# Kernel tuning notes

Hardware: AMD Instinct MI355X
Metric: run time of the kernel (lower is better)

## Reference

```python
import jax, jax.numpy as jnp
import numpy as np

B, S, IN, D, H, FF, L = 16, 1000, 32, 512, 8, 2048, 6
DK = D // H
EPS = 1e-5


def setup_inputs() -> dict:
    key = jax.random.key(0)
    ks = iter(jax.random.split(key, 64))
    def w(shape, s=0.02):
        return jax.random.normal(next(ks), shape, dtype=jnp.float32) * s
    inp = {
        'x': jax.random.normal(next(ks), (B, S, IN), dtype=jnp.float32),
        # input projection
        'Win': w((IN, D)), 'b_in': jnp.zeros((D,), jnp.float32),
        # per-layer attention weights (stacked over L layers)
        'Wq': w((L, D, D)), 'bq': jnp.zeros((L, D), jnp.float32),
        'Wk': w((L, D, D)), 'bk': jnp.zeros((L, D), jnp.float32),
        'Wv': w((L, D, D)), 'bv': jnp.zeros((L, D), jnp.float32),
        'Wo': w((L, D, D)), 'bo': jnp.zeros((L, D), jnp.float32),
        # per-layer feed-forward
        'W1': w((L, D, FF)), 'b1': jnp.zeros((L, FF), jnp.float32),
        'W2': w((L, FF, D)), 'b2': jnp.zeros((L, D), jnp.float32),
        # per-layer layernorms
        'ln1_g': jnp.ones((L, D), jnp.float32), 'ln1_b': jnp.zeros((L, D), jnp.float32),
        'ln2_g': jnp.ones((L, D), jnp.float32), 'ln2_b': jnp.zeros((L, D), jnp.float32),
        # final encoder norm
        'lnf_g': jnp.ones((D,), jnp.float32), 'lnf_b': jnp.zeros((D,), jnp.float32),
        # feature extraction head: D -> D/2 -> D/4
        'Wf1': w((D, D // 2)), 'bf1': jnp.zeros((D // 2,), jnp.float32),
        'Wf2': w((D // 2, D // 4)), 'bf2': jnp.zeros((D // 4,), jnp.float32),
        # reconstruction head: D/4 -> D/2 -> D -> IN
        'Wr1': w((D // 4, D // 2)), 'br1': jnp.zeros((D // 2,), jnp.float32),
        'Wr2': w((D // 2, D)), 'br2': jnp.zeros((D,), jnp.float32),
        'Wr3': w((D, IN)), 'br3': jnp.zeros((IN,), jnp.float32),
        # anomaly head: D/4 -> D/8 -> 1
        'Wa1': w((D // 4, D // 8)), 'ba1': jnp.zeros((D // 8,), jnp.float32),
        'Wa2': w((D // 8, 1)), 'ba2': jnp.zeros((1,), jnp.float32),
    }
    return inp


def _layernorm(x, g, b):
    m = jnp.mean(x, axis=-1, keepdims=True)
    v = jnp.var(x, axis=-1, keepdims=True)
    return (x - m) * jax.lax.rsqrt(v + EPS) * g + b


def _pos_encoding(seq_len, d_model):
    pos = jnp.arange(seq_len, dtype=jnp.float32)[:, None]
    div = jnp.exp(jnp.arange(0, d_model, 2, dtype=jnp.float32) * (-np.log(10000.0) / d_model))
    pe = jnp.zeros((seq_len, d_model), jnp.float32)
    pe = pe.at[:, 0::2].set(jnp.sin(pos * div))
    pe = pe.at[:, 1::2].set(jnp.cos(pos * div))
    return pe


def _encoder(h, Wq, bq, Wk, bk, Wv, bv, Wo, bo, W1, b1, W2, b2,
             ln1_g, ln1_b, ln2_g, ln2_b, lnf_g, lnf_b):
    h = h + _pos_encoding(h.shape[1], D)[None]
    scale = 1.0 / np.sqrt(DK)
    for i in range(L):
        # multi-head self-attention
        q = (h @ Wq[i] + bq[i]).reshape(B, S, H, DK).transpose(0, 2, 1, 3)
        k = (h @ Wk[i] + bk[i]).reshape(B, S, H, DK).transpose(0, 2, 1, 3)
        v = (h @ Wv[i] + bv[i]).reshape(B, S, H, DK).transpose(0, 2, 1, 3)
        scores = jnp.einsum('bhsd,bhtd->bhst', q, k) * scale  # [B,H,S,S]
        attn = jax.nn.softmax(scores, axis=-1)
        ctx = jnp.einsum('bhst,bhtd->bhsd', attn, v)
        ctx = ctx.transpose(0, 2, 1, 3).reshape(B, S, D)
        attn_out = ctx @ Wo[i] + bo[i]
        h = _layernorm(h + attn_out, ln1_g[i], ln1_b[i])
        # feed-forward
        ff = jax.nn.relu(h @ W1[i] + b1[i]) @ W2[i] + b2[i]
        h = _layernorm(h + ff, ln2_g[i], ln2_b[i])
    return _layernorm(h, lnf_g, lnf_b)


def reference(x, Win, b_in, Wq, bq, Wk, bk, Wv, bv, Wo, bo, W1, b1, W2, b2,
              ln1_g, ln1_b, ln2_g, ln2_b, lnf_g, lnf_b,
              Wf1, bf1, Wf2, bf2, Wr1, br1, Wr2, br2, Wr3, br3,
              Wa1, ba1, Wa2, ba2):
    h = x @ Win + b_in  # [B,S,D]
    h = _encoder(h, Wq, bq, Wk, bk, Wv, bv, Wo, bo, W1, b1, W2, b2,
                 ln1_g, ln1_b, ln2_g, ln2_b, lnf_g, lnf_b)
    feat = jax.nn.relu(h @ Wf1 + bf1) @ Wf2 + bf2  # [B,S,D/4]
    recon = jax.nn.relu(jax.nn.relu(feat @ Wr1 + br1) @ Wr2 + br2) @ Wr3 + br3  # [B,S,IN]
    anomaly = jax.nn.sigmoid(jax.nn.relu(feat @ Wa1 + ba1) @ Wa2 + ba2)  # [B,S,1]
    return recon, anomaly
```

## Files before the change

### kernel.cpp

```cpp
#include <hip/hip_runtime.h>
#include <hip/hip_bf16.h>
#include <math.h>

#define B_  16
#define S_  1000
#define IN_ 32
#define D_  512
#define H_  8
#define FF_ 2048
#define L_  6
#define DK_ 64
#define M_  (B_ * S_)
#define SP_ 1024

typedef __bf16 bf16x8 __attribute__((ext_vector_type(8)));
typedef float  floatx4 __attribute__((ext_vector_type(4)));

#define FLAG_RELU 1
#define FLAG_BF16 2
#define FLAG_QKV  4

#define QSCALE 0.18033688011112042f

__device__ __forceinline__ void gll16(const __bf16* g, __bf16* l) {
    __builtin_amdgcn_global_load_lds(
        (const __attribute__((address_space(1))) unsigned int*)g,
        (__attribute__((address_space(3))) unsigned int*)l, 16, 0, 0);
}

__global__ __launch_bounds__(256) void gemm_mfma(
    const __bf16* __restrict__ A, const __bf16* __restrict__ BT,
    const float* __restrict__ bias, void* __restrict__ C,
    int M, int N, int K, int flags)
{
    __shared__ __bf16 Asm[128 * 32];
    __shared__ __bf16 Bsm[128 * 32];

    int tid  = threadIdx.x;
    int wave = tid >> 6;
    int lane = tid & 63;
    int bm = blockIdx.y * 128;
    int bn = blockIdx.x * 128;
    int wm = (wave & 1) * 64;
    int wn = (wave >> 1) * 64;
    int lm = lane & 15;
    int lq = lane >> 4;

    floatx4 acc[4][4] = {};

    int crow  = tid >> 2;
    int cpart = (tid & 3) * 8;
    const __bf16* ag0 = A + (size_t)(bm + crow) * K + cpart;
    const __bf16* ag1 = A + (size_t)(bm + 64 + crow) * K + cpart;
    __bf16* al0 = Asm + tid * 8;
    __bf16* al1 = Asm + 2048 + tid * 8;
    int nr0 = bn + crow, nr1 = bn + 64 + crow;
    const __bf16* bg0 = BT + (size_t)nr0 * K + cpart;
    const __bf16* bg1 = BT + (size_t)nr1 * K + cpart;
    __bf16* bl0 = Bsm + tid * 8;
    __bf16* bl1 = Bsm + 2048 + tid * 8;
    bool bv0 = nr0 < N, bv1 = nr1 < N;

    for (int k0 = 0; k0 < K; k0 += 32) {
        __syncthreads();
        gll16(ag0 + k0, al0);
        gll16(ag1 + k0, al1);
        if (bv0) gll16(bg0 + k0, bl0);
        if (bv1) gll16(bg1 + k0, bl1);
        __syncthreads();

        bf16x8 af[4], bf[4];
        #pragma unroll
        for (int i = 0; i < 4; ++i) {
            af[i] = *(const bf16x8*)&Asm[(wm + i * 16 + lm) * 32 + lq * 8];
            bf[i] = *(const bf16x8*)&Bsm[(wn + i * 16 + lm) * 32 + lq * 8];
        }
        #pragma unroll
        for (int i = 0; i < 4; ++i)
            #pragma unroll
            for (int j = 0; j < 4; ++j)
                acc[i][j] = __builtin_amdgcn_mfma_f32_16x16x32_bf16(
                    af[i], bf[j], acc[i][j], 0, 0, 0);
    }

    if (flags & FLAG_QKV) {
        int sec = bn >> 9;
        if (sec < 2) {
            __bf16* dst = (__bf16*)C + (sec ? (size_t)8192000 : 0);
            #pragma unroll
            for (int j = 0; j < 4; ++j) {
                int col = (bn & 511) + wn + j * 16 + lm;
                float bvv = bias[bn + wn + j * 16 + lm];
                #pragma unroll
                for (int i = 0; i < 4; ++i)
                    #pragma unroll
                    for (int r = 0; r < 4; ++r) {
                        int m = bm + wm + i * 16 + lq * 4 + r;
                        dst[(size_t)m * 512 + col] = (__bf16)(acc[i][j][r] + bvv);
                    }
            }
        } else {
            __bf16* vt = (__bf16*)C + (size_t)16384000;
            int bbq[4], s0[4];
            #pragma unroll
            for (int i = 0; i < 4; ++i) {
                int m0 = bm + wm + i * 16 + lq * 4;
                bbq[i] = m0 / 1000;
                s0[i]  = m0 - bbq[i] * 1000;
            }
            #pragma unroll
            for (int j = 0; j < 4; ++j) {
                int col = (bn & 511) + wn + j * 16 + lm;
                float bvv = bias[bn + wn + j * 16 + lm];
                int head = col >> 6, dk = col & 63;
                #pragma unroll
                for (int i = 0; i < 4; ++i) {
                    __bf16 t4[4];
                    #pragma unroll
                    for (int r = 0; r < 4; ++r) t4[r] = (__bf16)(acc[i][j][r] + bvv);
                    *(uint2*)(vt + ((size_t)(bbq[i] * H_ + head) * DK_ + dk) * SP_ + s0[i])
                        = *(uint2*)t4;
                }
            }
        }
        return;
    }

    #pragma unroll
    for (int j = 0; j < 4; ++j) {
        int n = bn + wn + j * 16 + lm;
        if (n >= N) continue;
        float bv = bias[n];
        #pragma unroll
        for (int i = 0; i < 4; ++i) {
            #pragma unroll
            for (int r = 0; r < 4; ++r) {
                int m = bm + wm + i * 16 + lq * 4 + r;
                float v = acc[i][j][r] + bv;
                if (flags & FLAG_RELU) v = fmaxf(v, 0.f);
                if (flags & FLAG_BF16) ((__bf16*)C)[(size_t)m * N + n] = (__bf16)v;
                else                   ((float*)C)[(size_t)m * N + n] = v;
            }
        }
    }
}

__device__ __forceinline__ void trans_tile(
    const float* __restrict__ src, __bf16* __restrict__ dst,
    int K, int N, float scale, int tx0, int ty0)
{
    __shared__ float t[32][33];
    int n0 = tx0 * 32, k0 = ty0 * 32;
    int tx = threadIdx.x & 31, ty = threadIdx.x >> 5;
    #pragma unroll
    for (int i = 0; i < 32; i += 8) {
        int k = k0 + ty + i, n = n0 + tx;
        t[ty + i][tx] = (k < K && n < N) ? src[(size_t)k * N + n] * scale : 0.f;
    }
    __syncthreads();
    #pragma unroll
    for (int i = 0; i < 32; i += 8) {
        int n = n0 + ty + i, k = k0 + tx;
        if (n < N && k < K) dst[(size_t)n * K + k] = (__bf16)t[tx][ty + i];
    }
}

__global__ __launch_bounds__(256) void transpose_qkvo(
    const float* __restrict__ Wq, const float* __restrict__ Wk,
    const float* __restrict__ Wv, const float* __restrict__ Wo,
    __bf16* __restrict__ WqkvT, __bf16* __restrict__ WoT)
{
    int l = blockIdx.z >> 2, which = blockIdx.z & 3;
    const float* src; __bf16* dst; float sc = 1.f;
    size_t so = (size_t)l * 512 * 512;
    if (which == 0)      { src = Wq + so; dst = WqkvT + (size_t)l * 1536 * 512; sc = QSCALE; }
    else if (which == 1) { src = Wk + so; dst = WqkvT + (size_t)l * 1536 * 512 + 512 * 512; }
    else if (which == 2) { src = Wv + so; dst = WqkvT + (size_t)l * 1536 * 512 + 1024 * 512; }
    else                 { src = Wo + so; dst = WoT + so; }
    trans_tile(src, dst, 512, 512, sc, blockIdx.x, blockIdx.y);
}

__global__ __launch_bounds__(256) void transpose_ffn(
    const float* __restrict__ W1, const float* __restrict__ W2,
    __bf16* __restrict__ W1T, __bf16* __restrict__ W2T)
{
    int l = blockIdx.z >> 1, which = blockIdx.z & 1;
    size_t so = (size_t)l * 512 * 2048;
    int K = which ? 2048 : 512, N = which ? 512 : 2048;
    if ((int)blockIdx.x >= N / 32 || (int)blockIdx.y >= K / 32) return;
    trans_tile((which ? W2 : W1) + so, (which ? W2T : W1T) + so,
               K, N, 1.f, blockIdx.x, blockIdx.y);
}

struct TDesc { const float* src; __bf16* dst; int K; int N; float scale; };
struct TDescArr { TDesc d[7]; };

__global__ __launch_bounds__(256) void transpose_misc(TDescArr ds)
{
    TDesc t = ds.d[blockIdx.z];
    if ((int)blockIdx.x * 32 >= t.N || (int)blockIdx.y * 32 >= t.K) return;
    trans_tile(t.src, t.dst, t.K, t.N, t.scale, blockIdx.x, blockIdx.y);
}

__global__ void cast_bf16(const float* __restrict__ src, __bf16* __restrict__ dst, int n)
{
    int i = blockIdx.x * 256 + threadIdx.x;
    if (i < n) dst[i] = (__bf16)src[i];
}

__global__ void concat_bias(const float* __restrict__ bq, const float* __restrict__ bk,
                            const float* __restrict__ bv, float* __restrict__ dst)
{
    int i = blockIdx.x * 256 + threadIdx.x;
    if (i >= L_ * 1536) return;
    int l = i / 1536, j = i - l * 1536;
    float v = (j < 512) ? bq[l * 512 + j] * QSCALE
            : (j < 1024) ? bk[l * 512 + j - 512]
                         : bv[l * 512 + j - 1024];
    dst[i] = v;
}

__global__ void add_pos_kernel(float* __restrict__ h, __bf16* __restrict__ hb)
{
    int idx = blockIdx.x * 256 + threadIdx.x;
    if (idx >= B_ * S_ * D_) return;
    int d = idx % D_;
    int s = (idx / D_) % S_;
    int two_i = d & ~1;
    float ang = (float)s * expf((float)two_i * (-9.210340371976184f / (float)D_));
    float v = h[idx] + ((d & 1) ? cosf(ang) : sinf(ang));
    h[idx] = v;
    hb[idx] = (__bf16)v;
}

#define AST 72

__global__ __launch_bounds__(256) void attn_mfma(
    const __bf16* __restrict__ q, const __bf16* __restrict__ k,
    const __bf16* __restrict__ vt, __bf16* __restrict__ ctx)
{
    const int id = blockIdx.x;
    const int w  = (id & 7) * 128 + (id >> 3);
    const int qt = w & 7, hh = (w >> 3) & 7, bb = w >> 6;

    const int tid = threadIdx.x;
    const int wave = tid >> 6, lane = tid & 63;
    const int lm = lane & 15, lq = lane >> 4;

    __shared__ __bf16 Ks[64 * AST];
    __shared__ __bf16 Vt[64 * AST];

    const size_t headbase = (size_t)bb * S_ * D_ + hh * DK_;
    const __bf16* kbase  = k + headbase;
    const __bf16* vtbase = vt + (size_t)(bb * H_ + hh) * DK_ * SP_;

    bf16x8 af[2][2] = {};
    #pragma unroll
    for (int iq = 0; iq < 2; ++iq) {
        int qrow = qt * 128 + wave * 32 + iq * 16 + lm;
        if (qrow < S_) {
            const __bf16* qp = q + headbase + (size_t)qrow * D_;
            af[iq][0] = *(const bf16x8*)(qp + lq * 8);
            af[iq][1] = *(const bf16x8*)(qp + 32 + lq * 8);
        }
    }

    floatx4 oacc[2][4] = {};
    floatx4 lacc[2] = {};

    bf16x8 ones8;
    #pragma unroll
    for (int j = 0; j < 8; ++j) ones8[j] = (__bf16)1.f;

    const int sr  = tid >> 3;
    const int sc8 = (tid & 7) * 8;
    const int colA = (sc8 & 32) | ((sc8 & 8) << 1) | ((sc8 & 16) >> 2);

    uint4 ku[2], vu[2];
    #pragma unroll
    for (int i = 0; i < 2; ++i) {
        int r = sr + i * 32;
        ku[i] = *(const uint4*)(kbase + (size_t)r * D_ + sc8);
        vu[i] = *(const uint4*)(vtbase + (size_t)r * SP_ + sc8);
    }

    for (int jt = 0; jt < 16; ++jt) {
        const int t0 = jt * 64;
        const bool tail = (jt == 15);

        __syncthreads();
        #pragma unroll
        for (int i = 0; i < 2; ++i) {
            int r = sr + i * 32;
            *(uint4*)&Ks[r * AST + sc8] = ku[i];
            uint2 vlo = make_uint2(vu[i].x, vu[i].y);
            uint2 vhi = make_uint2(vu[i].z, vu[i].w);
            *(uint2*)&Vt[r * AST + colA]     = vlo;
            *(uint2*)&Vt[r * AST + colA + 8] = vhi;
        }
        __syncthreads();

        if (jt < 15) {
            int t0n = t0 + 64;
            #pragma unroll
            for (int i = 0; i < 2; ++i) {
                int r = sr + i * 32;
                int trow = t0n + r;
                ku[i] = (trow < S_) ? *(const uint4*)(kbase + (size_t)trow * D_ + sc8)
                                    : make_uint4(0, 0, 0, 0);
                vu[i] = *(const uint4*)(vtbase + (size_t)r * SP_ + t0n + sc8);
            }
        }

        #pragma unroll
        for (int iq = 0; iq < 2; ++iq) {
            floatx4 sacc[4] = {};
            #pragma unroll
            for (int ks = 0; ks < 2; ++ks)
                #pragma unroll
                for (int jb = 0; jb < 4; ++jb) {
                    bf16x8 kf = *(const bf16x8*)&Ks[(jb * 16 + lm) * AST + ks * 32 + lq * 8];
                    sacc[jb] = __builtin_amdgcn_mfma_f32_16x16x32_bf16(
                        kf, af[iq][ks], sacc[jb], 0, 0, 0);
                }

            bf16x8 pf[2];
            if (!tail) {
                #pragma unroll
                for (int jb = 0; jb < 4; ++jb)
                    #pragma unroll
                    for (int r = 0; r < 4; ++r)
                        pf[jb >> 1][(jb & 1) * 4 + r] = (__bf16)exp2f(sacc[jb][r]);
            } else {
                #pragma unroll
                for (int jb = 0; jb < 4; ++jb)
                    #pragma unroll
                    for (int r = 0; r < 4; ++r) {
                        bool valid = (t0 + jb * 16 + lq * 4 + r) < S_;
                        pf[jb >> 1][(jb & 1) * 4 + r] =
                            valid ? (__bf16)exp2f(sacc[jb][r]) : (__bf16)0.f;
                    }
            }

            #pragma unroll
            for (int ks = 0; ks < 2; ++ks) {
                #pragma unroll
                for (int jb = 0; jb < 4; ++jb) {
                    bf16x8 bvf = *(const bf16x8*)&Vt[(jb * 16 + lm) * AST + ks * 32 + lq * 8];
                    oacc[iq][jb] = __builtin_amdgcn_mfma_f32_16x16x32_bf16(
                        pf[ks], bvf, oacc[iq][jb], 0, 0, 0);
                }
                lacc[iq] = __builtin_amdgcn_mfma_f32_16x16x32_bf16(
                    pf[ks], ones8, lacc[iq], 0, 0, 0);
            }
        }
    }

    #pragma unroll
    for (int iq = 0; iq < 2; ++iq) {
        float linv[4];
        #pragma unroll
        for (int r = 0; r < 4; ++r)
            linv[r] = 1.f / lacc[iq][r];
        #pragma unroll
        for (int jb = 0; jb < 4; ++jb)
            #pragma unroll
            for (int r = 0; r < 4; ++r) {
                int srow = qt * 128 + wave * 32 + iq * 16 + lq * 4 + r;
                if (srow < S_)
                    ctx[headbase + (size_t)srow * D_ + jb * 16 + lm] =
                        (__bf16)(oacc[iq][jb][r] * linv[r]);
            }
    }
}

__global__ __launch_bounds__(256) void ln_kernel(
    const float* __restrict__ x, const __bf16* __restrict__ delta,
    const float* __restrict__ g, const float* __restrict__ b,
    float* __restrict__ out, __bf16* __restrict__ outb, int has_delta)
{
    int row = blockIdx.x;
    int tid = threadIdx.x;
    __shared__ float red[256];

    const size_t base = (size_t)row * D_;
    float v0 = x[base + tid];
    float v1 = x[base + tid + 256];
    if (has_delta) {
        v0 += (float)delta[base + tid];
        v1 += (float)delta[base + tid + 256];
    }
    red[tid] = v0 + v1; __syncthreads();
    for (int o = 128; o > 0; o >>= 1) {
        if (tid < o) red[tid] += red[tid + o];
        __syncthreads();
    }
    float mean = red[0] * (1.f / D_);
    __syncthreads();
    float d0 = v0 - mean, d1 = v1 - mean;
    red[tid] = d0 * d0 + d1 * d1; __syncthreads();
    for (int o = 128; o > 0; o >>= 1) {
        if (tid < o) red[tid] += red[tid + o];
        __syncthreads();
    }
    float rstd = rsqrtf(red[0] * (1.f / D_) + 1e-5f);
    float o0 = d0 * rstd * g[tid]       + b[tid];
    float o1 = d1 * rstd * g[tid + 256] + b[tid + 256];
    out[base + tid]        = o0;
    out[base + tid + 256]  = o1;
    outb[base + tid]       = (__bf16)o0;
    outb[base + tid + 256] = (__bf16)o1;
}

__global__ __launch_bounds__(256) void a2_kernel(
    const float* __restrict__ a1, const float* __restrict__ Wa2,
    const float* __restrict__ ba2, float* __restrict__ out)
{
    int row = blockIdx.x * 4 + (threadIdx.x >> 6);
    int lane = threadIdx.x & 63;
    if (row >= M_) return;
    float p = a1[(size_t)row * 64 + lane] * Wa2[lane];
    for (int o = 32; o > 0; o >>= 1) p += __shfl_down(p, o, 64);
    if (lane == 0) out[row] = 1.f / (1.f + expf(-(p + ba2[0])));
}

extern "C" void kernel_launch(void* const* d_in, const int* in_sizes, int n_in,
                              void* d_out, int out_size, void* d_ws, size_t ws_size,
                              hipStream_t stream)
{
    const float* x     = (const float*)d_in[0];
    const float* Win   = (const float*)d_in[1];
    const float* b_in  = (const float*)d_in[2];
    const float* Wq    = (const float*)d_in[3];
    const float* bq    = (const float*)d_in[4];
    const float* Wk    = (const float*)d_in[5];
    const float* bk    = (const float*)d_in[6];
    const float* Wv    = (const float*)d_in[7];
    const float* bv    = (const float*)d_in[8];
    const float* Wo    = (const float*)d_in[9];
    const float* bo    = (const float*)d_in[10];
    const float* W1    = (const float*)d_in[11];
    const float* b1    = (const float*)d_in[12];
    const float* W2    = (const float*)d_in[13];
    const float* b2    = (const float*)d_in[14];
    const float* ln1_g = (const float*)d_in[15];
    const float* ln1_b = (const float*)d_in[16];
    const float* ln2_g = (const float*)d_in[17];
    const float* ln2_b = (const float*)d_in[18];
    const float* lnf_g = (const float*)d_in[19];
    const float* lnf_b = (const float*)d_in[20];
    const float* Wf1   = (const float*)d_in[21];
    const float* bf1   = (const float*)d_in[22];
    const float* Wf2   = (const float*)d_in[23];
    const float* bf2   = (const float*)d_in[24];
    const float* Wr1   = (const float*)d_in[25];
    const float* br1   = (const float*)d_in[26];
    const float* Wr2   = (const float*)d_in[27];
    const float* br2   = (const float*)d_in[28];
    const float* Wr3   = (const float*)d_in[29];
    const float* br3   = (const float*)d_in[30];
    const float* Wa1   = (const float*)d_in[31];
    const float* ba1   = (const float*)d_in[32];
    const float* Wa2   = (const float*)d_in[33];
    const float* ba2   = (const float*)d_in[34];

    float* recon_out   = (float*)d_out;
    float* anomaly_out = (float*)d_out + (size_t)M_ * IN_;

    char* ws = (char*)d_ws;
    float*  h    = (float*)(ws + 0);
    __bf16* tmpb = (__bf16*)(ws + 32768000);
    __bf16* hb   = (__bf16*)(ws + 65536000);
    __bf16* qb   = (__bf16*)(ws + 81920000);
    __bf16* kb   = (__bf16*)(ws + 98304000);
    __bf16* vtb  = (__bf16*)(ws + 114688000);
    __bf16* ctxb = (__bf16*)(ws + 131465216);
    __bf16* ffmid = qb;

    __bf16* t1b   = (__bf16*)(ws + 81920000);
    __bf16* featb = (__bf16*)(ws + 90112000);
    __bf16* r1b   = (__bf16*)(ws + 94208000);
    __bf16* r2b   = (__bf16*)(ws + 102400000);
    float*  a1b   = (float*)(ws + 118784000);

    size_t woff = 147849216;
    auto alloc_bf = [&](size_t elems) { __bf16* p = (__bf16*)(ws + woff); woff += elems * 2; return p; };
    __bf16* WinT  = alloc_bf(32 * 512);
    __bf16* WqkvT = alloc_bf((size_t)L_ * 1536 * 512);
    __bf16* WoT   = alloc_bf((size_t)L_ * 512 * 512);
    __bf16* W1T   = alloc_bf((size_t)L_ * 512 * 2048);
    __bf16* W2T   = alloc_bf((size_t)L_ * 2048 * 512);
    __bf16* Wf1T  = alloc_bf(512 * 256);
    __bf16* Wf2T  = alloc_bf(256 * 128);
    __bf16* Wr1T  = alloc_bf(128 * 256);
    __bf16* Wr2T  = alloc_bf(256 * 512);
    __bf16* Wr3T  = alloc_bf(512 * 32);
    __bf16* Wa1T  = alloc_bf(128 * 64);
    __bf16* xb    = alloc_bf((size_t)M_ * IN_);
    float*  bqkv  = (float*)(ws + woff);  woff += (size_t)L_ * 1536 * 4;

    dim3 blk(256);
    auto gg = [](int N) { return dim3((N + 127) / 128, M_ / 128); };

    hipLaunchKernelGGL(transpose_qkvo, dim3(16, 16, L_ * 4), blk, 0, stream,
                       Wq, Wk, Wv, Wo, WqkvT, WoT);
    hipLaunchKernelGGL(transpose_ffn, dim3(64, 64, L_ * 2), blk, 0, stream,
                       W1, W2, W1T, W2T);
    TDescArr misc;
    misc.d[0] = {Win, WinT, 32, 512, 1.f};
    misc.d[1] = {Wf1, Wf1T, 512, 256, 1.f};
    misc.d[2] = {Wf2, Wf2T, 256, 128, 1.f};
    misc.d[3] = {Wr1, Wr1T, 128, 256, 1.f};
    misc.d[4] = {Wr2, Wr2T, 256, 512, 1.f};
    misc.d[5] = {Wr3, Wr3T, 512, 32, 1.f};
    misc.d[6] = {Wa1, Wa1T, 128, 64, 1.f};
    hipLaunchKernelGGL(transpose_misc, dim3(16, 16, 7), blk, 0, stream, misc);
    hipLaunchKernelGGL(cast_bf16, dim3((M_ * IN_ + 255) / 256), blk, 0, stream,
                       x, xb, M_ * IN_);
    hipLaunchKernelGGL(concat_bias, dim3((L_ * 1536 + 255) / 256), blk, 0, stream,
                       bq, bk, bv, bqkv);

    hipLaunchKernelGGL(gemm_mfma, gg(D_), blk, 0, stream,
                       xb, WinT, b_in, (void*)h, M_, D_, IN_, 0);
    hipLaunchKernelGGL(add_pos_kernel, dim3((B_ * S_ * D_ + 255) / 256), blk, 0, stream,
                       h, hb);

    for (int l = 0; l < L_; ++l) {
        size_t wo = (size_t)l * 512 * 512;
        size_t fo = (size_t)l * 512 * 2048;

        hipLaunchKernelGGL(gemm_mfma, dim3(12, M_ / 128), blk, 0, stream,
                           hb, WqkvT + (size_t)l * 1536 * 512, bqkv + (size_t)l * 1536,
                           (void*)qb, M_, 1536, 512, FLAG_QKV);

        hipLaunchKernelGGL(attn_mfma, dim3(1024), blk, 0, stream,
                           qb, kb, vtb, ctxb);

        hipLaunchKernelGGL(gemm_mfma, gg(D_), blk, 0, stream,
                           ctxb, WoT + wo, bo + (size_t)l * D_, (void*)tmpb, M_, D_, D_,
                           FLAG_BF16);
        hipLaunchKernelGGL(ln_kernel, dim3(M_), blk, 0, stream,
                           h, tmpb, ln1_g + (size_t)l * D_, ln1_b + (size_t)l * D_, h, hb, 1);

        hipLaunchKernelGGL(gemm_mfma, gg(FF_), blk, 0, stream,
                           hb, W1T + fo, b1 + (size_t)l * FF_, (void*)ffmid, M_, FF_, D_,
                           FLAG_RELU | FLAG_BF16);
        hipLaunchKernelGGL(gemm_mfma, gg(D_), blk, 0, stream,
                           ffmid, W2T + fo, b2 + (size_t)l * D_, (void*)tmpb, M_, D_, FF_,
                           FLAG_BF16);
        hipLaunchKernelGGL(ln_kernel, dim3(M_), blk, 0, stream,
                           h, tmpb, ln2_g + (size_t)l * D_, ln2_b + (size_t)l * D_, h, hb, 1);
    }

    hipLaunchKernelGGL(ln_kernel, dim3(M_), blk, 0, stream,
                       h, nullptr, lnf_g, lnf_b, h, hb, 0);

    hipLaunchKernelGGL(gemm_mfma, gg(256), blk, 0, stream,
                       hb, Wf1T, bf1, (void*)t1b, M_, 256, 512, FLAG_RELU | FLAG_BF16);
    hipLaunchKernelGGL(gemm_mfma, gg(128), blk, 0, stream,
                       t1b, Wf2T, bf2, (void*)featb, M_, 128, 256, FLAG_BF16);

    hipLaunchKernelGGL(gemm_mfma, gg(256), blk, 0, stream,
                       featb, Wr1T, br1, (void*)r1b, M_, 256, 128, FLAG_RELU | FLAG_BF16);
    hipLaunchKernelGGL(gemm_mfma, gg(512), blk, 0, stream,
                       r1b, Wr2T, br2, (void*)r2b, M_, 512, 256, FLAG_RELU | FLAG_BF16);
    hipLaunchKernelGGL(gemm_mfma, gg(IN_), blk, 0, stream,
                       r2b, Wr3T, br3, (void*)recon_out, M_, IN_, 512, 0);

    hipLaunchKernelGGL(gemm_mfma, gg(64), blk, 0, stream,
                       featb, Wa1T, ba1, (void*)a1b, M_, 64, 128, FLAG_RELU);
    hipLaunchKernelGGL(a2_kernel, dim3((M_ + 3) / 4), blk, 0, stream,
                       a1b, Wa2, ba2, anomaly_out);
}
```

Measured before the change: 1.989 ms.

## Double-buffer GEMM LDS tiles with register prefetch instead of direct global-to-LDS loads

Replaces the global_load_lds path in the MFMA GEMM with register-staged loads into two LDS buffers. The next K-tile is fetched into registers while the current tile is consumed, which drops one barrier per iteration and overlaps global latency with MFMA work. This doubles LDS use and adds register pressure, and it gives up the direct global-to-LDS path.

Measured after the change: 1.959 ms. No clear change (-1.5%).

```diff
diff --git a/kernel.cpp b/kernel.cpp
--- a/kernel.cpp
+++ b/kernel.cpp
@@ -22,19 +22,13 @@
 
 #define QSCALE 0.18033688011112042f
 
-__device__ __forceinline__ void gll16(const __bf16* g, __bf16* l) {
-    __builtin_amdgcn_global_load_lds(
-        (const __attribute__((address_space(1))) unsigned int*)g,
-        (__attribute__((address_space(3))) unsigned int*)l, 16, 0, 0);
-}
-
 __global__ __launch_bounds__(256) void gemm_mfma(
     const __bf16* __restrict__ A, const __bf16* __restrict__ BT,
     const float* __restrict__ bias, void* __restrict__ C,
     int M, int N, int K, int flags)
 {
-    __shared__ __bf16 Asm[128 * 32];
-    __shared__ __bf16 Bsm[128 * 32];
+    __shared__ __bf16 Asm[2][128 * 32];
+    __shared__ __bf16 Bsm[2][128 * 32];
 
     int tid  = threadIdx.x;
     int wave = tid >> 6;
@@ -52,28 +46,37 @@
     int cpart = (tid & 3) * 8;
     const __bf16* ag0 = A + (size_t)(bm + crow) * K + cpart;
     const __bf16* ag1 = A + (size_t)(bm + 64 + crow) * K + cpart;
-    __bf16* al0 = Asm + tid * 8;
-    __bf16* al1 = Asm + 2048 + tid * 8;
     int nr0 = bn + crow, nr1 = bn + 64 + crow;
     const __bf16* bg0 = BT + (size_t)nr0 * K + cpart;
     const __bf16* bg1 = BT + (size_t)nr1 * K + cpart;
-    __bf16* bl0 = Bsm + tid * 8;
-    __bf16* bl1 = Bsm + 2048 + tid * 8;
     bool bv0 = nr0 < N, bv1 = nr1 < N;
 
-    for (int k0 = 0; k0 < K; k0 += 32) {
+    uint4 pa0, pa1, pb0, pb1;
+    pa0 = *(const uint4*)ag0;
+    pa1 = *(const uint4*)ag1;
+    pb0 = bv0 ? *(const uint4*)bg0 : make_uint4(0, 0, 0, 0);
+    pb1 = bv1 ? *(const uint4*)bg1 : make_uint4(0, 0, 0, 0);
+
+    for (int k0 = 0, it = 0; k0 < K; k0 += 32, ++it) {
+        const int cur = it & 1;
+        *(uint4*)&Asm[cur][tid * 8]        = pa0;
+        *(uint4*)&Asm[cur][2048 + tid * 8] = pa1;
+        *(uint4*)&Bsm[cur][tid * 8]        = pb0;
+        *(uint4*)&Bsm[cur][2048 + tid * 8] = pb1;
         __syncthreads();
-        gll16(ag0 + k0, al0);
-        gll16(ag1 + k0, al1);
-        if (bv0) gll16(bg0 + k0, bl0);
-        if (bv1) gll16(bg1 + k0, bl1);
-        __syncthreads();
+
+        if (k0 + 32 < K) {
+            pa0 = *(const uint4*)(ag0 + k0 + 32);
+            pa1 = *(const uint4*)(ag1 + k0 + 32);
+            pb0 = bv0 ? *(const uint4*)(bg0 + k0 + 32) : make_uint4(0, 0, 0, 0);
+            pb1 = bv1 ? *(const uint4*)(bg1 + k0 + 32) : make_uint4(0, 0, 0, 0);
+        }
 
         bf16x8 af[4], bf[4];
         #pragma unroll
         for (int i = 0; i < 4; ++i) {
-            af[i] = *(const bf16x8*)&Asm[(wm + i * 16 + lm) * 32 + lq * 8];
-            bf[i] = *(const bf16x8*)&Bsm[(wn + i * 16 + lm) * 32 + lq * 8];
+            af[i] = *(const bf16x8*)&Asm[cur][(wm + i * 16 + lm) * 32 + lq * 8];
+            bf[i] = *(const bf16x8*)&Bsm[cur][(wn + i * 16 + lm) * 32 + lq * 8];
         }
         #pragma unroll
         for (int i = 0; i < 4; ++i)
```
